# Kernel tuning notes

Hardware: AMD Instinct MI355X
Metric: run time of the kernel (lower is better)

The kernel has to match this reference:

```python
import jax, jax.numpy as jnp
import numpy as np
from jax import lax

NEG = -1e30  # log-space 'zero' that stays finite for stable grads


def _logadd3(a, b, c):
    m = jnp.maximum(jnp.maximum(a, b), c)
    return m + jnp.log(jnp.exp(a - m) + jnp.exp(b - m) + jnp.exp(c - m))


def _logadd2(a, b):
    m = jnp.maximum(a, b)
    return m + jnp.log(jnp.exp(a - m) + jnp.exp(b - m))


def setup_inputs() -> dict:
    key = jax.random.key(0)
    k1, k2, k3 = jax.random.split(key, 3)
    B, T, V, L = 64, 2000, 512, 200
    logits = jax.random.normal(k1, (B, T, V), dtype=jnp.float32)
    # keep input lengths well above 2*L+1 so all paths are feasible
    input_lengths = (T - jax.random.randint(k2, (B,), 0, 256)).astype(jnp.int32)
    targets = jax.random.randint(k3, (B, L), 0, V, dtype=jnp.int32)  # 0 == pad == blank
    return {"logits": logits, "input_lengths": input_lengths, "targets": targets}


def ctc_loss_sum(logits, input_lengths, targets):
    B, T, V = logits.shape
    L = targets.shape[1]
    S = 2 * L + 1

    lp = jax.nn.log_softmax(logits, axis=-1)  # [B,T,V]

    # compact nonzero targets per row (masked_select equivalent, fixed shape)
    mask = targets != 0
    tlen = mask.sum(-1)  # [B] target_lengths
    pos = jnp.where(mask, jnp.cumsum(mask, axis=1) - 1, L)
    compact = jnp.zeros_like(targets).at[jnp.arange(B)[:, None], pos].set(targets, mode="drop")

    # extended label sequence: blank, y1, blank, y2, ..., blank  -> [B,S]
    s_idx = jnp.arange(S)
    lab_idx = jnp.clip((s_idx - 1) // 2, 0, L - 1)
    ext = jnp.where(s_idx % 2 == 1, compact[:, lab_idx], 0)  # [B,S]

    # skip transition s-2 -> s allowed iff label at s is non-blank and differs from s-2
    ext_m2 = jnp.pad(ext, ((0, 0), (2, 0)))[:, :S]
    skip_ok = (ext != 0) & (ext != ext_m2) & (s_idx >= 2)  # [B,S]

    lpT = jnp.transpose(lp, (1, 0, 2))  # [T,B,V], scan over time

    # init: alpha_0[0]=lp(blank), alpha_0[1]=lp(y1)
    lp0_ext = jnp.take_along_axis(lpT[0], ext[:, :2], axis=1)  # [B,2]
    alpha0 = jnp.full((B, S), NEG, dtype=lp.dtype).at[:, :2].set(lp0_ext)

    def step(alpha, inp):
        lp_t, t = inp
        a1 = jnp.pad(alpha, ((0, 0), (1, 0)), constant_values=NEG)[:, :S]
        a2 = jnp.pad(alpha, ((0, 0), (2, 0)), constant_values=NEG)[:, :S]
        a2 = jnp.where(skip_ok, a2, NEG)
        lp_e = jnp.take_along_axis(lp_t, ext, axis=1)  # [B,S]
        new = _logadd3(alpha, a1, a2) + lp_e
        active = (t < input_lengths)[:, None]
        return jnp.where(active, new, alpha), None

    alphaT, _ = lax.scan(step, alpha0, (lpT[1:], jnp.arange(1, T)))

    # read out at final blank (2*tlen) and final label (2*tlen-1)
    e1 = (2 * tlen)[:, None]
    e2 = (2 * tlen - 1)
    a1 = jnp.take_along_axis(alphaT, e1, axis=1)[:, 0]
    a2 = jnp.where(e2 >= 0,
                   jnp.take_along_axis(alphaT, jnp.clip(e2, 0)[:, None], axis=1)[:, 0],
                   NEG)
    ll = _logadd2(a1, a2)  # [B] log p(targets | logits)
    return -jnp.sum(ll)


def reference(logits, input_lengths, targets):
    return ctc_loss_sum(logits, input_lengths, targets)
```

## Files before the change

kernel.cpp:

```cpp
#include <hip/hip_runtime.h>

#define B_ 64
#define T_ 2000
#define V_ 512
#define L_ 200
#define NCONS 128
#define NPRODB (B_ * 250)


typedef _Float16 half4 __attribute__((ext_vector_type(4)));
union H4U { unsigned long long u; half4 h; float2 f2; };

__device__ __forceinline__ float dpp_shr1_f(float x) {
  return __int_as_float(__builtin_amdgcn_update_dpp(0, __float_as_int(x), 0x138, 0xf, 0xf, true));
}
__device__ __forceinline__ int dpp_shr1_i(int x) {
  return __builtin_amdgcn_update_dpp(0, x, 0x138, 0xf, 0xf, true);
}
__device__ __forceinline__ float dpp_shl1_f(float x) {
  return __int_as_float(__builtin_amdgcn_update_dpp(0, __float_as_int(x), 0x130, 0xf, 0xf, true));
}
__device__ __forceinline__ int dpp_shl1_i(int x) {
  return __builtin_amdgcn_update_dpp(0, x, 0x130, 0xf, 0xf, true);
}
#define DPPADD(v, ctrl, rmask)                                                              \
  v += __int_as_float(__builtin_amdgcn_update_dpp(0, __float_as_int(v), ctrl, rmask, 0xf, true));

__device__ __forceinline__ int ldflag(const int* p) {
  return __hip_atomic_load(p, __ATOMIC_RELAXED, __HIP_MEMORY_SCOPE_AGENT);
}

__global__ __launch_bounds__(64) void kflags(int* __restrict__ flags) {
  const int base = blockIdx.x * 256 + threadIdx.x;
  flags[base] = 0; flags[base + 64] = 0; flags[base + 128] = 0; flags[base + 192] = 0;
}

__global__ __launch_bounds__(64, 2) void ctc_split(
    const float* __restrict__ logits, const int* __restrict__ lens,
    const int* __restrict__ targets, unsigned long long* __restrict__ cull,
    unsigned long long* __restrict__ bull, int* __restrict__ flags,
    float* __restrict__ AF, int* __restrict__ EF,
    float* __restrict__ DD, int* __restrict__ EB) {
  const int lane = threadIdx.x;
  __shared__ int cmp[256];
  __shared__ __align__(16) float scr[2][512];

#define COMPACT(BB)                                                          \
  int base = 0;                                                              \
  {                                                                          \
    cmp[lane] = 0; cmp[64 + lane] = 0; cmp[128 + lane] = 0; cmp[192 + lane] = 0; \
    _Pragma("unroll") for (int cc = 0; cc < 4; ++cc) {                       \
      const int l = cc * 64 + lane;                                          \
      const int v = (l < L_) ? targets[(BB) * L_ + l] : 0;                   \
      const unsigned long long mk = __ballot(v != 0);                        \
      const int pos = base + __popcll(mk & ((1ull << lane) - 1ull));         \
      if (v != 0) cmp[pos] = v;                                              \
      base += __popcll(mk);                                                  \
    }                                                                        \
    asm volatile("s_waitcnt lgkmcnt(0)" ::: "memory");                       \
  }

  if ((int)blockIdx.x >= NCONS) {
    const int g = blockIdx.x - NCONS;
    const int b = g & 63;
    const int j = g >> 6;
    const int len = lens[b];
    const int nch = (len + 7) >> 3;
    if (j >= nch) return;
    const int c = (j & 1) ? (nch - 1 - (j >> 1)) : (j >> 1);

    COMPACT(b);
    const int4 c4 = *(const int4*)(&cmp[4 * lane]);
    const int l0 = 4 * lane;
    const bool v0 = l0 + 0 < L_, v1 = l0 + 1 < L_, v2 = l0 + 2 < L_, v3 = l0 + 3 < L_;

    const float* rowp = logits + (size_t)b * (T_ * V_) + (size_t)c * (8 * V_);
    float4 X[16];
#pragma unroll
    for (int r = 0; r < 8; ++r) {
      X[2 * r] = *(const float4*)(rowp + r * V_ + 4 * lane);
      X[2 * r + 1] = *(const float4*)(rowp + r * V_ + 256 + 4 * lane);
    }
    const size_t obase = ((size_t)(b * T_ + c * 8)) * 64 + lane;
#pragma unroll
    for (int r = 0; r < 8; ++r) {
      const float4 xe = X[2 * r], xo = X[2 * r + 1];
      const float e0 = __expf(xe.x), e1 = __expf(xe.y), e2 = __expf(xe.z), e3 = __expf(xe.w);
      const float e4 = __expf(xo.x), e5 = __expf(xo.y), e6 = __expf(xo.z), e7 = __expf(xo.w);
      float s = ((e0 + e1) + (e2 + e3)) + ((e4 + e5) + (e6 + e7));
      DPPADD(s, 0x111, 0xf); DPPADD(s, 0x112, 0xf); DPPADD(s, 0x114, 0xf);
      DPPADD(s, 0x118, 0xf); DPPADD(s, 0x142, 0xa); DPPADD(s, 0x143, 0xc);
      const float sum = __int_as_float(__builtin_amdgcn_readlane(__float_as_int(s), 63));
      const float inv = 32.0f / sum;
      float* sc = &scr[r & 1][0];
      *(float4*)(sc + 4 * lane) = make_float4(e0, e1, e2, e3);
      *(float4*)(sc + 256 + 4 * lane) = make_float4(e4, e5, e6, e7);
      asm volatile("s_waitcnt lgkmcnt(0)" ::: "memory");
      H4U p;
      p.h.x = (_Float16)(v0 ? sc[c4.x] * inv : 0.0f);
      p.h.y = (_Float16)(v1 ? sc[c4.y] * inv : 0.0f);
      p.h.z = (_Float16)(v2 ? sc[c4.z] * inv : 0.0f);
      p.h.w = (_Float16)(v3 ? sc[c4.w] * inv : 0.0f);
      __hip_atomic_store(cull + obase + (size_t)r * 64, p.u, __ATOMIC_RELAXED,
                         __HIP_MEMORY_SCOPE_AGENT);
      if (lane == 0) {
        unsigned* b32 = (unsigned*)bull;
        __hip_atomic_store(b32 + b * 2048 + c * 8 + r, __float_as_uint(e0 * inv),
                           __ATOMIC_RELAXED, __HIP_MEMORY_SCOPE_AGENT);
      }
    }
    asm volatile("s_waitcnt vmcnt(0)" ::: "memory");
    if (lane == 0)
      __hip_atomic_store(flags + b * 256 + c, 1, __ATOMIC_RELAXED, __HIP_MEMORY_SCOPE_AGENT);
    return;
  }

  const int b = blockIdx.x >> 1;
  const int dirb = blockIdx.x & 1;
  const int len = lens[b];
  const int rem = len & 7;
  const int nch = (len + 7) >> 3;
  const int Cf = nch >> 1;
  const int Ntot = dirb ? (nch - Cf) : Cf;
  const int c0v = dirb ? (nch - 1) : 0;
  const int dstep = dirb ? -1 : 1;
#define CHK(J) (c0v + dstep * (J))

  COMPACT(b);
  const int tl = base;
  const int4 c4 = *(const int4*)(&cmp[4 * lane]);

  const int cm1 = __shfl_up(c4.w, 1);
  const float m0 = (lane > 0 && c4.x != 0 && c4.x != cm1) ? 1.0f : 0.0f;
  const float m1 = (c4.y != 0 && c4.y != c4.x) ? 1.0f : 0.0f;
  const float m2 = (c4.z != 0 && c4.z != c4.y) ? 1.0f : 0.0f;
  const float m3 = (c4.w != 0 && c4.w != c4.z) ? 1.0f : 0.0f;
  const float m0n = dpp_shl1_f(m0);

  float a0 = 0.f, a1 = 0.f, a2 = 0.f, a3 = 0.f, a4 = 0.f, a5 = 0.f, a6 = 0.f, a7 = 0.f;
  int E = 0;
  float fac = 1.0f;
  if (!dirb) {
    if (lane == 0) a0 = 1.0f;
  } else {
    const int st = 2 * tl;
    if (lane == (st >> 3)) {
      const int e = st & 7;
      a0 = (e == 0) ? 1.0f : 0.0f; a1 = (e == 1) ? 1.0f : 0.0f;
      a2 = (e == 2) ? 1.0f : 0.0f; a3 = (e == 3) ? 1.0f : 0.0f;
      a4 = (e == 4) ? 1.0f : 0.0f; a5 = (e == 5) ? 1.0f : 0.0f;
      a6 = (e == 6) ? 1.0f : 0.0f; a7 = (e == 7) ? 1.0f : 0.0f;
    }
  }
  __builtin_amdgcn_s_setprio(1);

  unsigned long long LB0[8], LB1[8], LB2[8], LB3[8];
  float4 BLa0, BLb0, BLa1, BLb1, BLa2, BLb2, BLa3, BLb3;

#define POLL(CIDX)                                                           \
  {                                                                          \
    int* fp_ = flags + b * 256 + (CIDX);                                     \
    while (ldflag(fp_) == 0) __builtin_amdgcn_s_sleep(2);                    \
    asm volatile("" ::: "memory");                                           \
  }

#define LOADC(S, CIDX)                                                       \
  {                                                                          \
    const int c_ = (CIDX);                                                   \
    const size_t base_ = ((size_t)(b * T_ + c_ * 8)) * 64 + lane;            \
    _Pragma("unroll") for (int u = 0; u < 8; ++u)                            \
        LB##S[u] = __hip_atomic_load(cull + base_ + (size_t)u * 64,          \
                                     __ATOMIC_RELAXED, __HIP_MEMORY_SCOPE_AGENT); \
    const size_t bb_ = (size_t)b * 1024 + (size_t)c_ * 4;                    \
    H4U t0_, t1_, t2_, t3_;                                                  \
    t0_.u = __hip_atomic_load(bull + bb_ + 0, __ATOMIC_RELAXED, __HIP_MEMORY_SCOPE_AGENT); \
    t1_.u = __hip_atomic_load(bull + bb_ + 1, __ATOMIC_RELAXED, __HIP_MEMORY_SCOPE_AGENT); \
    t2_.u = __hip_atomic_load(bull + bb_ + 2, __ATOMIC_RELAXED, __HIP_MEMORY_SCOPE_AGENT); \
    t3_.u = __hip_atomic_load(bull + bb_ + 3, __ATOMIC_RELAXED, __HIP_MEMORY_SCOPE_AGENT); \
    BLa##S = make_float4(t0_.f2.x, t0_.f2.y, t1_.f2.x, t1_.f2.y);            \
    BLb##S = make_float4(t2_.f2.x, t2_.f2.y, t3_.f2.x, t3_.f2.y);            \
  }

#define PREFETCH(S)                                                          \
  {                                                                          \
    const int nx_ = i + 4;                                                   \
    if (nx_ < Ntot) {                                                        \
      if (nf0 == 0) POLL(CHK(nx_));                                          \
      LOADC(S, CHK(nx_));                                                    \
      nf0 = nf1;                                                             \
      const int n2_ = nx_ + 2;                                               \
      nf1 = (n2_ < Ntot) ? ldflag(flags + b * 256 + CHK(n2_)) : 1;           \
    }                                                                        \
  }

#define STEP8F(S)                                                            \
  {                                                                          \
    const float blv_[8] = {BLa##S.x, BLa##S.y, BLa##S.z, BLa##S.w,           \
                           BLb##S.x, BLb##S.y, BLb##S.z, BLb##S.w};          \
    _Pragma("unroll") for (int u = 0; u < 8; ++u) {                          \
      H4U q_; q_.u = LB##S[u];                                               \
      const float qx = (float)q_.h.x, qy = (float)q_.h.y;                    \
      const float qz = (float)q_.h.z, qw = (float)q_.h.w;                    \
      const float pbv = blv_[u];                                             \
      const float s1 = dpp_shr1_f(a7) * fac;                 \
      float n0 = (a0 + s1) * pbv;                                            \
      float n1 = fmaf(m0, s1, a0 + a1) * qx;                                 \
      float n2 = (a2 + a1) * pbv;                                            \
      float n3 = fmaf(m1, a1, a2 + a3) * qy;                                 \
      float n4 = (a4 + a3) * pbv;                                            \
      float n5 = fmaf(m2, a3, a4 + a5) * qz;                                 \
      float n6 = (a6 + a5) * pbv;                                            \
      float n7 = fmaf(m3, a5, a6 + a7) * qw;                                 \
      a0 = n0; a1 = n1; a2 = n2; a3 = n3;                                    \
      a4 = n4; a5 = n5; a6 = n6; a7 = n7;                                    \
    }                                                                        \
  }

#define STEP8B(S, UHI)                                                       \
  {                                                                          \
    const float blv_[8] = {BLa##S.x, BLa##S.y, BLa##S.z, BLa##S.w,           \
                           BLb##S.x, BLb##S.y, BLb##S.z, BLb##S.w};          \
    _Pragma("unroll") for (int u = 7; u >= 0; --u) {                         \
      if (u <= (UHI)) {                                                      \
        H4U q_; q_.u = LB##S[u];                                             \
        const float qx = (float)q_.h.x, qy = (float)q_.h.y;                  \
        const float qz = (float)q_.h.z, qw = (float)q_.h.w;                  \
        const float pbv = blv_[u];                                           \
        const float sa = dpp_shl1_f(a0) * fac;              \
        const float sb = dpp_shl1_f(a1) * fac;                               \
        float n0 = (a0 + a1) * pbv;                                          \
        float n1 = fmaf(m1, a3, a1 + a2) * qx;                               \
        float n2 = (a2 + a3) * pbv;                                          \
        float n3 = fmaf(m2, a5, a3 + a4) * qy;                               \
        float n4 = (a4 + a5) * pbv;                                          \
        float n5 = fmaf(m3, a7, a5 + a6) * qz;                               \
        float n6 = (a6 + a7) * pbv;                                          \
        float n7 = fmaf(m0n, sb, a7 + sa) * qw;                              \
        a0 = n0; a1 = n1; a2 = n2; a3 = n3;                                  \
        a4 = n4; a5 = n5; a6 = n6; a7 = n7;                                  \
      }                                                                      \
    }                                                                        \
  }

#define RENORM_COMMON                                                        \
    const float mx = fmaxf(fmaxf(fmaxf(a0, a1), fmaxf(a2, a3)),              \
                           fmaxf(fmaxf(a4, a5), fmaxf(a6, a7)));             \
    const bool dead = (mx == 0.0f);                                          \
    int e_ = (int)((__float_as_uint(mx) >> 23) & 0xff) - 127;                \
    if (dead) e_ = 0;                                                        \
    const float sc_ = __int_as_float((unsigned)(127 - e_) << 23);            \
    a0 *= sc_; a1 *= sc_; a2 *= sc_; a3 *= sc_;                              \
    a4 *= sc_; a5 *= sc_; a6 *= sc_; a7 *= sc_;                              \
    const int En_ = E + e_;

#define RENORMF                                                              \
  {                                                                          \
    RENORM_COMMON                                                            \
    const int EnP_ = dpp_shr1_i(En_);                                        \
    E = dead ? EnP_ : En_;                                                   \
    const int Ep_ = dpp_shr1_i(E);                                           \
    const int d_ = Ep_ - E;                                                  \
    int dc_ = d_ < -126 ? -126 : (d_ > 126 ? 126 : d_);                      \
    fac = (d_ < -126) ? 0.0f : __int_as_float((unsigned)(dc_ + 127) << 23);  \
  }

#define RENORMB                                                              \
  {                                                                          \
    RENORM_COMMON                                                            \
    const int EnP_ = dpp_shl1_i(En_);                                        \
    E = dead ? EnP_ : En_;                                                   \
    const int Ep_ = dpp_shl1_i(E);                                           \
    const int d_ = Ep_ - E;                                                  \
    int dc_ = d_ < -126 ? -126 : (d_ > 126 ? 126 : d_);                      \
    fac = (d_ < -126) ? 0.0f : __int_as_float((unsigned)(dc_ + 127) << 23);  \
  }

  POLL(CHK(0)); LOADC(0, CHK(0));
  POLL(CHK(1)); LOADC(1, CHK(1));
  POLL(CHK(2)); LOADC(2, CHK(2));
  POLL(CHK(3)); LOADC(3, CHK(3));
  int nf0 = (4 < Ntot) ? ldflag(flags + b * 256 + CHK(4)) : 1;
  int nf1 = (5 < Ntot) ? ldflag(flags + b * 256 + CHK(5)) : 1;

  if (!dirb) {
    for (int i = 0; i < Ntot; ++i) {
      switch (i & 3) {
        case 0: STEP8F(0); RENORMF; PREFETCH(0); break;
        case 1: STEP8F(1); RENORMF; PREFETCH(1); break;
        case 2: STEP8F(2); RENORMF; PREFETCH(2); break;
        default: STEP8F(3); RENORMF; PREFETCH(3); break;
      }
    }
    *(float4*)(AF + b * 512 + lane * 8) = make_float4(a0, a1, a2, a3);
    *(float4*)(AF + b * 512 + lane * 8 + 4) = make_float4(a4, a5, a6, a7);
    EF[b * 64 + lane] = E;
  } else {
    for (int i = 0; i < Ntot; ++i) {
      const int uh = (i == 0 && rem) ? (rem - 1) : 7;
      switch (i & 3) {
        case 0: STEP8B(0, uh); RENORMB; PREFETCH(0); break;
        case 1: STEP8B(1, uh); RENORMB; PREFETCH(1); break;
        case 2: STEP8B(2, uh); RENORMB; PREFETCH(2); break;
        default: STEP8B(3, uh); RENORMB; PREFETCH(3); break;
      }
    }
    const float sa = dpp_shl1_f(a0) * fac;
    const float sb = dpp_shl1_f(a1) * fac;
    const float d0 = a0 + a1;
    const float d1 = fmaf(m1, a3, a1 + a2);
    const float d2 = a2 + a3;
    const float d3 = fmaf(m2, a5, a3 + a4);
    const float d4 = a4 + a5;
    const float d5 = fmaf(m3, a7, a5 + a6);
    const float d6 = a6 + a7;
    const float d7 = fmaf(m0n, sb, a7 + sa);
    *(float4*)(DD + b * 512 + lane * 8) = make_float4(d0, d1, d2, d3);
    *(float4*)(DD + b * 512 + lane * 8 + 4) = make_float4(d4, d5, d6, d7);
    EB[b * 64 + lane] = E;
  }
#undef POLL
#undef LOADC
#undef PREFETCH
#undef STEP8F
#undef STEP8B
#undef RENORM_COMMON
#undef RENORMF
#undef RENORMB
#undef COMPACT
#undef CHK
}

__global__ __launch_bounds__(512) void kcomb(const int* __restrict__ lens,
                                             const float* __restrict__ AF,
                                             const int* __restrict__ EF,
                                             const float* __restrict__ DD,
                                             const int* __restrict__ EB,
                                             float* __restrict__ out) {
  const int wid = threadIdx.x >> 6;
  const int lane = threadIdx.x & 63;
  __shared__ float part[8];
  float acc = 0.0f;
#pragma unroll
  for (int q = 0; q < 8; ++q) {
    const int b = wid * 8 + q;
    const float4 f0 = *(const float4*)(AF + b * 512 + lane * 8);
    const float4 f1 = *(const float4*)(AF + b * 512 + lane * 8 + 4);
    const float4 g0 = *(const float4*)(DD + b * 512 + lane * 8);
    const float4 g1 = *(const float4*)(DD + b * 512 + lane * 8 + 4);
    const float dot = ((f0.x * g0.x + f0.y * g0.y) + (f0.z * g0.z + f0.w * g0.w)) +
                      ((f1.x * g1.x + f1.y * g1.y) + (f1.z * g1.z + f1.w * g1.w));
    const int Es = EF[b * 64 + lane] + EB[b * 64 + lane];
    const bool z = (dot == 0.0f);
    int Ek = z ? (-(1 << 28)) : Es;
#pragma unroll
    for (int off = 32; off; off >>= 1) {
      const int o = __shfl_xor(Ek, off);
      Ek = o > Ek ? o : Ek;
    }
    float v = z ? 0.0f : ldexpf(dot, Es - Ek);
#pragma unroll
    for (int off = 32; off; off >>= 1) v += __shfl_xor(v, off);
    const float ll = __logf(v) + (float)Ek * 0.69314718056f - (float)lens[b] * 3.46573590280f;
    acc -= ll;
  }
  if (lane == 0) part[wid] = acc;
  __syncthreads();
  if (threadIdx.x == 0) {
    float s = ((part[0] + part[1]) + (part[2] + part[3])) +
              ((part[4] + part[5]) + (part[6] + part[7]));
    out[0] = s;
  }
}

extern "C" void kernel_launch(void* const* d_in, const int* in_sizes, int n_in,
                              void* d_out, int out_size, void* d_ws, size_t ws_size,
                              hipStream_t stream) {
  const float* logits = (const float*)d_in[0];
  const int* input_lengths = (const int*)d_in[1];
  const int* targets = (const int*)d_in[2];
  float* out = (float*)d_out;
  unsigned long long* cull = (unsigned long long*)d_ws;
  unsigned long long* bull = (unsigned long long*)((char*)d_ws + 65536000);
  int* flags = (int*)((char*)d_ws + 66060288);
  float* AF = (float*)((char*)d_ws + 66125824);
  int* EF = (int*)((char*)d_ws + 66256896);
  float* DD = (float*)((char*)d_ws + 66273280);
  int* EB = (int*)((char*)d_ws + 66404352);
  (void)in_sizes; (void)n_in; (void)out_size; (void)ws_size;

  kflags<<<B_, 64, 0, stream>>>(flags);
  ctc_split<<<NCONS + NPRODB, 64, 0, stream>>>(logits, input_lengths, targets,
                                               cull, bull, flags, AF, EF, DD, EB);
  kcomb<<<1, 512, 0, stream>>>(input_lengths, AF, EF, DD, EB, out);
}
```

Baseline: 486.1 us.

## Pack four producer waves per block and use release-store flags

Producer blocks now have 256 threads, with four waves each handling one time chunk. Target compaction is done once per block in LDS, and the block count drops from 250 to 63 per batch row. Per-element atomic stores become plain stores, and the readiness flag is published with a release store in place of an explicit vmcnt wait. Consumer blocks also launch with 256 threads but keep only wave 0, which wastes slots and may change occupancy for the long-running consumer waves.

```diff
diff --git a/kernel.cpp b/kernel.cpp
--- a/kernel.cpp
+++ b/kernel.cpp
@@ -5,7 +5,8 @@
 #define V_ 512
 #define L_ 200
 #define NCONS 128
-#define NPRODB (B_ * 250)
+#define NJB 63
+#define NPRODB (B_ * NJB)
 
 
 typedef _Float16 half4 __attribute__((ext_vector_type(4)));
@@ -35,15 +36,17 @@
   flags[base] = 0; flags[base + 64] = 0; flags[base + 128] = 0; flags[base + 192] = 0;
 }
 
-__global__ __launch_bounds__(64, 2) void ctc_split(
+__global__ __launch_bounds__(256, 2) void ctc_split(
     const float* __restrict__ logits, const int* __restrict__ lens,
     const int* __restrict__ targets, unsigned long long* __restrict__ cull,
     unsigned long long* __restrict__ bull, int* __restrict__ flags,
     float* __restrict__ AF, int* __restrict__ EF,
     float* __restrict__ DD, int* __restrict__ EB) {
-  const int lane = threadIdx.x;
+  const int tid = threadIdx.x;
+  const int wid = tid >> 6;
+  const int lane = tid & 63;
   __shared__ int cmp[256];
-  __shared__ __align__(16) float scr[2][512];
+  __shared__ __align__(16) float scr[4][2][512];
 
 #define COMPACT(BB)                                                          \
   int base = 0;                                                              \
@@ -63,58 +66,56 @@
   if ((int)blockIdx.x >= NCONS) {
     const int g = blockIdx.x - NCONS;
     const int b = g & 63;
-    const int j = g >> 6;
+    const int jb = g >> 6;
     const int len = lens[b];
     const int nch = (len + 7) >> 3;
-    if (j >= nch) return;
-    const int c = (j & 1) ? (nch - 1 - (j >> 1)) : (j >> 1);
-
-    COMPACT(b);
-    const int4 c4 = *(const int4*)(&cmp[4 * lane]);
-    const int l0 = 4 * lane;
-    const bool v0 = l0 + 0 < L_, v1 = l0 + 1 < L_, v2 = l0 + 2 < L_, v3 = l0 + 3 < L_;
-
-    const float* rowp = logits + (size_t)b * (T_ * V_) + (size_t)c * (8 * V_);
-    float4 X[16];
-#pragma unroll
-    for (int r = 0; r < 8; ++r) {
-      X[2 * r] = *(const float4*)(rowp + r * V_ + 4 * lane);
-      X[2 * r + 1] = *(const float4*)(rowp + r * V_ + 256 + 4 * lane);
-    }
-    const size_t obase = ((size_t)(b * T_ + c * 8)) * 64 + lane;
-#pragma unroll
-    for (int r = 0; r < 8; ++r) {
-      const float4 xe = X[2 * r], xo = X[2 * r + 1];
-      const float e0 = __expf(xe.x), e1 = __expf(xe.y), e2 = __expf(xe.z), e3 = __expf(xe.w);
-      const float e4 = __expf(xo.x), e5 = __expf(xo.y), e6 = __expf(xo.z), e7 = __expf(xo.w);
-      float s = ((e0 + e1) + (e2 + e3)) + ((e4 + e5) + (e6 + e7));
-      DPPADD(s, 0x111, 0xf); DPPADD(s, 0x112, 0xf); DPPADD(s, 0x114, 0xf);
-      DPPADD(s, 0x118, 0xf); DPPADD(s, 0x142, 0xa); DPPADD(s, 0x143, 0xc);
-      const float sum = __int_as_float(__builtin_amdgcn_readlane(__float_as_int(s), 63));
-      const float inv = 32.0f / sum;
-      float* sc = &scr[r & 1][0];
-      *(float4*)(sc + 4 * lane) = make_float4(e0, e1, e2, e3);
-      *(float4*)(sc + 256 + 4 * lane) = make_float4(e4, e5, e6, e7);
-      asm volatile("s_waitcnt lgkmcnt(0)" ::: "memory");
-      H4U p;
-      p.h.x = (_Float16)(v0 ? sc[c4.x] * inv : 0.0f);
-      p.h.y = (_Float16)(v1 ? sc[c4.y] * inv : 0.0f);
-      p.h.z = (_Float16)(v2 ? sc[c4.z] * inv : 0.0f);
-      p.h.w = (_Float16)(v3 ? sc[c4.w] * inv : 0.0f);
-      __hip_atomic_store(cull + obase + (size_t)r * 64, p.u, __ATOMIC_RELAXED,
-                         __HIP_MEMORY_SCOPE_AGENT);
-      if (lane == 0) {
-        unsigned* b32 = (unsigned*)bull;
-        __hip_atomic_store(b32 + b * 2048 + c * 8 + r, __float_as_uint(e0 * inv),
-                           __ATOMIC_RELAXED, __HIP_MEMORY_SCOPE_AGENT);
+    if (wid == 0) { COMPACT(b); }
+    __syncthreads();
+    const int j = jb * 4 + wid;
+    if (j < nch) {
+      const int c = (j & 1) ? (nch - 1 - (j >> 1)) : (j >> 1);
+      const int4 c4 = *(const int4*)(&cmp[4 * lane]);
+      const int l0 = 4 * lane;
+      const bool v0 = l0 + 0 < L_, v1 = l0 + 1 < L_, v2 = l0 + 2 < L_, v3 = l0 + 3 < L_;
+
+      const float* rowp = logits + (size_t)b * (T_ * V_) + (size_t)c * (8 * V_);
+      float4 X[16];
+#pragma unroll
+      for (int r = 0; r < 8; ++r) {
+        X[2 * r] = *(const float4*)(rowp + r * V_ + 4 * lane);
+        X[2 * r + 1] = *(const float4*)(rowp + r * V_ + 256 + 4 * lane);
       }
-    }
-    asm volatile("s_waitcnt vmcnt(0)" ::: "memory");
-    if (lane == 0)
-      __hip_atomic_store(flags + b * 256 + c, 1, __ATOMIC_RELAXED, __HIP_MEMORY_SCOPE_AGENT);
+      const size_t obase = ((size_t)(b * T_ + c * 8)) * 64 + lane;
+#pragma unroll
+      for (int r = 0; r < 8; ++r) {
+        const float4 xe = X[2 * r], xo = X[2 * r + 1];
+        const float e0 = __expf(xe.x), e1 = __expf(xe.y), e2 = __expf(xe.z), e3 = __expf(xe.w);
+        const float e4 = __expf(xo.x), e5 = __expf(xo.y), e6 = __expf(xo.z), e7 = __expf(xo.w);
+        float s = ((e0 + e1) + (e2 + e3)) + ((e4 + e5) + (e6 + e7));
+        DPPADD(s, 0x111, 0xf); DPPADD(s, 0x112, 0xf); DPPADD(s, 0x114, 0xf);
+        DPPADD(s, 0x118, 0xf); DPPADD(s, 0x142, 0xa); DPPADD(s, 0x143, 0xc);
+        const float sum = __int_as_float(__builtin_amdgcn_readlane(__float_as_int(s), 63));
+        const float inv = 32.0f / sum;
+        float* sc = &scr[wid][r & 1][0];
+        *(float4*)(sc + 4 * lane) = make_float4(e0, e1, e2, e3);
+        *(float4*)(sc + 256 + 4 * lane) = make_float4(e4, e5, e6, e7);
+        asm volatile("s_waitcnt lgkmcnt(0)" ::: "memory");
+        H4U p;
+        p.h.x = (_Float16)(v0 ? sc[c4.x] * inv : 0.0f);
+        p.h.y = (_Float16)(v1 ? sc[c4.y] * inv : 0.0f);
+        p.h.z = (_Float16)(v2 ? sc[c4.z] * inv : 0.0f);
+        p.h.w = (_Float16)(v3 ? sc[c4.w] * inv : 0.0f);
+        cull[obase + (size_t)r * 64] = p.u;
+        if (lane == 0)
+          ((unsigned*)bull)[b * 2048 + c * 8 + r] = __float_as_uint(e0 * inv);
+      }
+      if (lane == 0)
+        __hip_atomic_store(flags + b * 256 + c, 1, __ATOMIC_RELEASE, __HIP_MEMORY_SCOPE_AGENT);
+    }
     return;
   }
 
+  if (wid != 0) return;
   const int b = blockIdx.x >> 1;
   const int dirb = blockIdx.x & 1;
   const int len = lens[b];
@@ -389,7 +390,7 @@
   (void)in_sizes; (void)n_in; (void)out_size; (void)ws_size;
 
   kflags<<<B_, 64, 0, stream>>>(flags);
-  ctc_split<<<NCONS + NPRODB, 64, 0, stream>>>(logits, input_lengths, targets,
-                                               cull, bull, flags, AF, EF, DD, EB);
+  ctc_split<<<NCONS + NPRODB, 256, 0, stream>>>(logits, input_lengths, targets,
+                                                cull, bull, flags, AF, EF, DD, EB);
   kcomb<<<1, 512, 0, stream>>>(input_lengths, AF, EF, DD, EB, out);
 }
```

After: 1.066 ms. 2.19x slower.
